# Performance work log

Hardware: AMD Instinct MI355X
Metric: run time of the kernel (lower is better)

The kernel has to match this reference:

```python
import jax, jax.numpy as jnp
import numpy as np
import math

B, S, H, NH = 1, 2048, 1024, 16  # batch, seq, hidden, heads


def setup_inputs() -> dict:
    key = jax.random.key(0)
    ks = jax.random.split(key, 12)
    inp = {
        "query": jax.random.normal(ks[0], (B, S, H), dtype=jnp.float32),
        "key": jax.random.normal(ks[1], (B, S, H), dtype=jnp.float32),
        "value": jax.random.normal(ks[2], (B, S, H), dtype=jnp.float32),
        "attention_mask": jax.random.randint(ks[3], (1, 1, S, S), 0, 2, dtype=jnp.int32),
        # torch nn.Linear params: y = x @ W.T + b, W init ~ U(-1/sqrt(H), 1/sqrt(H))
        "Wq": jax.random.uniform(ks[4], (H, H), jnp.float32, -1, 1) / math.sqrt(H),
        "bq": jax.random.uniform(ks[5], (H,), jnp.float32, -1, 1) / math.sqrt(H),
        "Wk": jax.random.uniform(ks[6], (H, H), jnp.float32, -1, 1) / math.sqrt(H),
        "bk": jax.random.uniform(ks[7], (H,), jnp.float32, -1, 1) / math.sqrt(H),
        "Wv": jax.random.uniform(ks[8], (H, H), jnp.float32, -1, 1) / math.sqrt(H),
        "bv": jax.random.uniform(ks[9], (H,), jnp.float32, -1, 1) / math.sqrt(H),
        "Wo": jax.random.uniform(ks[10], (H, H), jnp.float32, -1, 1) / math.sqrt(H),
        "bo": jax.random.uniform(ks[11], (H,), jnp.float32, -1, 1) / math.sqrt(H),
        "head": NH,
        "hidden_size": H,
    }
    return inp


def reference(query, key, value, attention_mask, Wq, bq, Wk, bk, Wv, bv, Wo, bo, head, hidden_size):
    b, s, _ = query.shape
    d_k = hidden_size // head

    def proj(x, W, bias):
        # [b, s, hidden] -> [b, head, s, d_k]
        y = x @ W.T + bias
        return y.reshape(b, s, head, d_k).transpose(0, 2, 1, 3)

    q = proj(query, Wq, bq)
    k = proj(key, Wk, bk)
    v = proj(value, Wv, bv)

    # naive full score matrix, as in the source (scale by sqrt(d_k) = last dim of q)
    scores = jnp.einsum("bhqd,bhkd->bhqk", q, k) / math.sqrt(d_k)
    # faithful quirk: masked positions are set to 0 (not -inf) before softmax
    scores = jnp.where(attention_mask == 0, jnp.zeros((), scores.dtype), scores)
    attn = jax.nn.softmax(scores, axis=-1)

    out = jnp.einsum("bhqk,bhkd->bhqd", attn, v)  # [b, head, s, d_k]
    out = out.transpose(0, 2, 1, 3).reshape(b, s, head * d_k)
    return out @ Wo.T + bo
```

## Files before the change

kernel.cpp:

```cpp
#include <hip/hip_runtime.h>
#include <hip/hip_bf16.h>


#define S_LEN 2048
#define HID   1024
#define NHEAD 16
#define DK    64

typedef unsigned short u16;
typedef __attribute__((ext_vector_type(8))) short bf16x8;
typedef __attribute__((ext_vector_type(4))) short bf16x4;
typedef __attribute__((ext_vector_type(4))) float f32x4;
typedef __attribute__((ext_vector_type(4))) unsigned u32x4;

__device__ __forceinline__ void load16_lds(const void* g, void* l) {
  __builtin_amdgcn_global_load_lds(
      (const __attribute__((address_space(1))) void*)g,
      (__attribute__((address_space(3))) void*)l, 16, 0, 0);
}

__device__ __forceinline__ short bfbits(float x) {
  __hip_bfloat16 h = __float2bfloat16(x);
  return *(short*)&h;
}
__device__ __forceinline__ bf16x8 cvt8(float4 a, float4 b) {
  bf16x8 r;
  r[0] = bfbits(a.x); r[1] = bfbits(a.y); r[2] = bfbits(a.z); r[3] = bfbits(a.w);
  r[4] = bfbits(b.x); r[5] = bfbits(b.y); r[6] = bfbits(b.z); r[7] = bfbits(b.w);
  return r;
}
__device__ __forceinline__ float bf2f(u16 u) {
  unsigned v = (unsigned)u << 16;
  return *(float*)&v;
}

__global__ __launch_bounds__(256) void cvt_kernel(
    const float* __restrict__ q, const float* __restrict__ k,
    const float* __restrict__ v, const float* __restrict__ wq,
    const float* __restrict__ wk, const float* __restrict__ wv,
    const float* __restrict__ wo, u16* __restrict__ Xbf,
    u16* __restrict__ Wbf) {
  const int y = blockIdx.y;
  size_t i = ((size_t)blockIdx.x * 256 + threadIdx.x) * 8;
  const float* src;
  u16* dst;
  size_t n;
  if (y < 3) {
    src = y == 0 ? q : (y == 1 ? k : v);
    dst = Xbf + (size_t)y * (S_LEN * HID);
    n = (size_t)S_LEN * HID;
  } else {
    int w = y - 3;
    src = w == 0 ? wq : (w == 1 ? wk : (w == 2 ? wv : wo));
    dst = Wbf + (size_t)w * (HID * HID);
    n = (size_t)HID * HID;
  }
  if (i >= n) return;
  float4 a = *(const float4*)(src + i);
  float4 b = *(const float4*)(src + i + 4);
  *(bf16x8*)(dst + i) = cvt8(a, b);
}

__global__ __launch_bounds__(256) void pack_mask_kernel(
    const int* __restrict__ mask, unsigned int* __restrict__ bitsT) {
  int idx = blockIdx.x * 256 + threadIdx.x;
  int row = idx & 2047, widx = idx >> 11;
  const int4* p = (const int4*)(mask + (size_t)row * S_LEN + widx * 32);
  unsigned word = 0;
#pragma unroll
  for (int i = 0; i < 8; ++i) {
    int4 v = p[i];
    word |= (unsigned)(v.x != 0) << (i * 4 + 0);
    word |= (unsigned)(v.y != 0) << (i * 4 + 1);
    word |= (unsigned)(v.z != 0) << (i * 4 + 2);
    word |= (unsigned)(v.w != 0) << (i * 4 + 3);
  }
  bitsT[(size_t)widx * S_LEN + row] = word;
}

__global__ __launch_bounds__(256) void gemm_qkv(
    const u16* __restrict__ Xbf, const u16* __restrict__ Wbf,
    const float* __restrict__ bq, const float* __restrict__ bk,
    const float* __restrict__ bv, u16* __restrict__ Qb,
    u16* __restrict__ Kb, u16* __restrict__ Vt) {
  constexpr int Mm = 2048, Nn = 1024, Kk = 1024, NIT = 16;
  const int z = blockIdx.z;
  const u16* A = Xbf + (size_t)z * (S_LEN * HID);
  const u16* W = Wbf + (size_t)z * (HID * HID);
  const float* bias = z == 0 ? bq : (z == 1 ? bk : bv);
  u16* C = z == 0 ? Qb : (z == 1 ? Kb : Vt);
  const float oscale = (z == 0) ? 0.125f * 1.44269504088896f : 1.0f;
  const int transpose = (z == 2);

  const int tid = threadIdx.x, lane = tid & 63, wave = tid >> 6;
  const int q4 = lane >> 4, c16 = lane & 15;
  const int bx = blockIdx.x;
  const int xcd = bx & 7, sIdx = bx >> 3;
  const int mBase = ((xcd >> 1) * 8 + (sIdx & 7)) * 64;
  const int nBase = ((xcd & 1) * 4 + (sIdx >> 3)) * 128;
  const int wn = wave * 32;

  __shared__ __align__(16) u16 As[2][2][64 * 32];
  __shared__ __align__(16) u16 Bs[2][2][128 * 32];

  f32x4 acc[4][2] = {};
  const int srow = lane >> 2;
  const int sx8 = ((lane & 3) ^ ((srow >> 1) & 3)) * 8;
  const int rx8 = (q4 ^ ((c16 >> 1) & 3)) * 8;

  auto issue = [&](int it, int buf) {
#pragma unroll
    for (int j = 0; j < 2; ++j) {
      int u = wave * 2 + j, h = u >> 2, grp = u & 3;
      load16_lds(A + (size_t)(mBase + grp * 16 + srow) * Kk + it * 64 +
                     h * 32 + sx8,
                 &As[buf][h][grp * 512]);
    }
#pragma unroll
    for (int j = 0; j < 4; ++j) {
      int u = wave * 4 + j, h = u >> 3, grp = u & 7;
      load16_lds(W + (size_t)(nBase + grp * 16 + srow) * Kk + it * 64 +
                     h * 32 + sx8,
                 &Bs[buf][h][grp * 512]);
    }
  };

  issue(0, 0);
  __syncthreads();

  for (int it = 0; it < NIT; ++it) {
    const int buf = it & 1, nbuf = buf ^ 1;
    if (it + 1 < NIT) issue(it + 1, nbuf);
#pragma unroll
    for (int kk = 0; kk < 2; ++kk) {
      bf16x8 af[4], bfr[2];
#pragma unroll
      for (int t = 0; t < 4; ++t)
        af[t] = *(const bf16x8*)&As[buf][kk][(t * 16 + c16) * 32 + rx8];
#pragma unroll
      for (int t = 0; t < 2; ++t)
        bfr[t] = *(const bf16x8*)&Bs[buf][kk][(wn + t * 16 + c16) * 32 + rx8];
#pragma unroll
      for (int mt = 0; mt < 4; ++mt)
#pragma unroll
        for (int nt = 0; nt < 2; ++nt)
          acc[mt][nt] = __builtin_amdgcn_mfma_f32_16x16x32_bf16(
              af[mt], bfr[nt], acc[mt][nt], 0, 0, 0);
    }
    __syncthreads();
  }

#pragma unroll
  for (int nt = 0; nt < 2; ++nt) {
    int col = nBase + wn + nt * 16 + c16;
    float bv2 = bias[col];
#pragma unroll
    for (int mt = 0; mt < 4; ++mt) {
#pragma unroll
      for (int r = 0; r < 4; ++r) {
        int row = mBase + mt * 16 + q4 * 4 + r;
        float v = (acc[mt][nt][r] + bv2) * oscale;
        if (transpose) {
          int vv = row & 31;
          int rowp = (row & ~31) | (((vv & 15) << 1) | (vv >> 4));
          ((__hip_bfloat16*)C)[(size_t)col * Mm + rowp] = __float2bfloat16(v);
        } else {
          ((__hip_bfloat16*)C)[(size_t)row * Nn + col] = __float2bfloat16(v);
        }
      }
    }
  }
}

__global__ __launch_bounds__(512, 4) void attn_kernel(
    const u16* __restrict__ Qb, const u16* __restrict__ Kb,
    const u16* __restrict__ Vt, const unsigned* __restrict__ mbT,
    u16* __restrict__ partOA, u16* __restrict__ partO3,
    float* __restrict__ partL) {
  constexpr int NITA = 8;
  const int lin = blockIdx.x + 8 * (blockIdx.y + 16 * blockIdx.z);
  const int work = ((lin & 7) << 6) | (lin >> 3);
  const int qt = work & 7, h = (work >> 3) & 15, zz = work >> 7;
  const int tid = threadIdx.x, lane = tid & 63, wave = tid >> 6;
  const int q4 = lane >> 4, c16 = lane & 15;

  __shared__ __align__(16) u16 Ks[2][2][64 * 32];
  __shared__ __align__(16) u16 Vs[2][2][64 * 32];
  __shared__ __align__(16) u16 Ps[8][32 * 72];

  const int q0 = qt * 256 + wave * 32;

  bf16x8 qf[2][2];
#pragma unroll
  for (int m = 0; m < 2; ++m)
#pragma unroll
    for (int kk = 0; kk < 2; ++kk)
      qf[m][kk] = *(const bf16x8*)(Qb + (size_t)(q0 + m * 16 + c16) * HID +
                                   h * DK + kk * 32 + q4 * 8);

  f32x4 o[2][4] = {};
  float l_lane[2][4] = {{}, {}};
  const unsigned mlo = 1u << c16, mhi = mlo << 16;

  const int srow = lane >> 2;
  const int sx8 = ((lane & 3) ^ ((srow >> 1) & 3)) * 8;
  const int rx8 = (q4 ^ ((c16 >> 1) & 3)) * 8;
  const int kvbase = zz * (S_LEN / 4);

  auto issueKV = [&](int it, int buf) {
    const int kv0 = kvbase + it * 64;
#pragma unroll
    for (int j = 0; j < 2; ++j) {
      int i = wave * 2 + j;
      if (i < 8) {
        int half = i >> 2, grp = i & 3;
        load16_lds(Kb + (size_t)(kv0 + grp * 16 + srow) * HID + h * DK +
                       half * 32 + sx8,
                   &Ks[buf][half][grp * 512]);
      } else {
        int ii = i - 8;
        int half = ii >> 2, grp = ii & 3;
        load16_lds(Vt + (size_t)(h * DK + grp * 16 + srow) * S_LEN + kv0 +
                       half * 32 + sx8,
                   &Vs[buf][half][grp * 512]);
      }
    }
  };

  issueKV(0, 0);
  __syncthreads();

  u16* pw = &Ps[wave][0];

  for (int it = 0; it < NITA; ++it) {
    const int buf = it & 1, nbuf = buf ^ 1;
    if (it + 1 < NITA) issueKV(it + 1, nbuf);

    const unsigned* mr = mbT + (size_t)(zz * 16 + it * 2) * S_LEN + q0 + q4 * 4;
    u32x4 mwa[2][2];
#pragma unroll
    for (int m = 0; m < 2; ++m) {
      mwa[m][0] = *(const u32x4*)(mr + m * 16);
      mwa[m][1] = *(const u32x4*)(mr + S_LEN + m * 16);
    }

    f32x4 sv[2][4];
#pragma unroll
    for (int nt = 0; nt < 4; ++nt) {
      const int rsw = (nt * 16 + c16) * 32 + rx8;
      bf16x8 kf0 = *(const bf16x8*)&Ks[buf][0][rsw];
      bf16x8 kf1 = *(const bf16x8*)&Ks[buf][1][rsw];
#pragma unroll
      for (int m = 0; m < 2; ++m) {
        f32x4 a = {};
        a = __builtin_amdgcn_mfma_f32_16x16x32_bf16(qf[m][0], kf0, a, 0, 0, 0);
        a = __builtin_amdgcn_mfma_f32_16x16x32_bf16(qf[m][1], kf1, a, 0, 0, 0);
        sv[m][nt] = a;
      }
    }

#pragma unroll
    for (int m = 0; m < 2; ++m)
#pragma unroll
      for (int r = 0; r < 4; ++r) {
#pragma unroll
        for (int nt = 0; nt < 4; ++nt) {
          unsigned word = mwa[m][nt >> 1][r];
          unsigned keep = word & ((nt & 1) ? mhi : mlo);
          float s = keep ? sv[m][nt][r] : 0.0f;
          float p = exp2f(s);
          sv[m][nt][r] = p;
          l_lane[m][r] += p;
        }
        int prow = m * 16 + q4 * 4 + r;
#pragma unroll
        for (int kkp = 0; kkp < 2; ++kkp) {
          unsigned lo = (unsigned)(u16)bfbits(sv[m][2 * kkp][r]);
          unsigned hi = (unsigned)(u16)bfbits(sv[m][2 * kkp + 1][r]);
          *(unsigned*)&pw[prow * 72 + kkp * 32 + c16 * 2] = lo | (hi << 16);
        }
      }

    asm volatile("s_waitcnt lgkmcnt(0)" ::: "memory");

#pragma unroll
    for (int kk = 0; kk < 2; ++kk) {
      bf16x8 pa0 = *(const bf16x8*)&pw[(c16) * 72 + kk * 32 + q4 * 8];
      bf16x8 pa1 = *(const bf16x8*)&pw[(16 + c16) * 72 + kk * 32 + q4 * 8];
#pragma unroll
      for (int nt = 0; nt < 4; ++nt) {
        const int rsw = (nt * 16 + c16) * 32 + rx8;
        bf16x8 vb = *(const bf16x8*)&Vs[buf][kk][rsw];
        o[0][nt] = __builtin_amdgcn_mfma_f32_16x16x32_bf16(pa0, vb, o[0][nt], 0, 0, 0);
        o[1][nt] = __builtin_amdgcn_mfma_f32_16x16x32_bf16(pa1, vb, o[1][nt], 0, 0, 0);
      }
    }
    __syncthreads();
  }

  u16* pO = (zz < 3) ? (partOA + (size_t)zz * (S_LEN * HID)) : partO3;
#pragma unroll
  for (int m = 0; m < 2; ++m)
#pragma unroll
    for (int r = 0; r < 4; ++r) {
      float s = l_lane[m][r];
#pragma unroll
      for (int d = 1; d < 16; d <<= 1) s += __shfl_xor(s, d);
      int row = q0 + m * 16 + q4 * 4 + r;
#pragma unroll
      for (int nt = 0; nt < 4; ++nt)
        ((__hip_bfloat16*)pO)[(size_t)row * HID + h * DK + nt * 16 + c16] =
            __float2bfloat16(o[m][nt][r]);
      if (c16 == 0)
        partL[((size_t)zz * NHEAD + h) * S_LEN + row] = s;
    }
}

__global__ __launch_bounds__(256) void combine_kernel(
    const u16* __restrict__ pOA, const u16* __restrict__ pO3,
    const float* __restrict__ partL, u16* __restrict__ ctx) {
  size_t idx = ((size_t)blockIdx.x * 256 + threadIdx.x) * 4;
  int row = (int)(idx >> 10);
  int col = (int)(idx & 1023);
  int h = col >> 6;
  float l = 0.0f;
#pragma unroll
  for (int z = 0; z < 4; ++z)
    l += partL[((size_t)z * NHEAD + h) * S_LEN + row];
  float inv = 1.0f / l;
  bf16x4 a0 = *(const bf16x4*)(pOA + idx);
  bf16x4 a1 = *(const bf16x4*)(pOA + (size_t)S_LEN * HID + idx);
  bf16x4 a2 = *(const bf16x4*)(pOA + 2 * (size_t)S_LEN * HID + idx);
  bf16x4 a3 = *(const bf16x4*)(pO3 + idx);
  bf16x4 r;
#pragma unroll
  for (int j = 0; j < 4; ++j) {
    float v = (bf2f((u16)a0[j]) + bf2f((u16)a1[j]) + bf2f((u16)a2[j]) +
               bf2f((u16)a3[j])) * inv;
    r[j] = bfbits(v);
  }
  *(bf16x4*)(ctx + idx) = r;
}

__global__ __launch_bounds__(256) void gemm_out(
    const u16* __restrict__ ctx, const u16* __restrict__ Wo,
    const float* __restrict__ bo, float* __restrict__ out) {
  constexpr int Nn = 1024, Kk = 1024, NIT = 16;
  const int tid = threadIdx.x, lane = tid & 63, wave = tid >> 6;
  const int q4 = lane >> 4, c16 = lane & 15;
  const int bx = blockIdx.x;
  const int xcd = bx & 7, sIdx = bx >> 3;
  const int mBase = ((xcd >> 1) * 16 + (sIdx & 15)) * 32;
  const int nBase = ((xcd & 1) * 4 + (sIdx >> 4)) * 128;
  const int wn = wave * 32;

  __shared__ __align__(16) u16 As[2][2][32 * 32];
  __shared__ __align__(16) u16 Bs[2][2][128 * 32];

  f32x4 acc[2][2] = {};
  const int srow = lane >> 2;
  const int sx8 = ((lane & 3) ^ ((srow >> 1) & 3)) * 8;
  const int rx8 = (q4 ^ ((c16 >> 1) & 3)) * 8;

  auto issue = [&](int it, int buf) {
    {
      int u = wave, h = u >> 1, grp = u & 1;
      load16_lds(ctx + (size_t)(mBase + grp * 16 + srow) * Kk + it * 64 +
                     h * 32 + sx8,
                 &As[buf][h][grp * 512]);
    }
#pragma unroll
    for (int j = 0; j < 4; ++j) {
      int u = wave * 4 + j, h = u >> 3, grp = u & 7;
      load16_lds(Wo + (size_t)(nBase + grp * 16 + srow) * Kk + it * 64 +
                     h * 32 + sx8,
                 &Bs[buf][h][grp * 512]);
    }
  };

  issue(0, 0);
  __syncthreads();

  for (int it = 0; it < NIT; ++it) {
    const int buf = it & 1, nbuf = buf ^ 1;
    if (it + 1 < NIT) issue(it + 1, nbuf);
#pragma unroll
    for (int kk = 0; kk < 2; ++kk) {
      bf16x8 af[2], bfr[2];
#pragma unroll
      for (int t = 0; t < 2; ++t)
        af[t] = *(const bf16x8*)&As[buf][kk][(t * 16 + c16) * 32 + rx8];
#pragma unroll
      for (int t = 0; t < 2; ++t)
        bfr[t] = *(const bf16x8*)&Bs[buf][kk][(wn + t * 16 + c16) * 32 + rx8];
#pragma unroll
      for (int mt = 0; mt < 2; ++mt)
#pragma unroll
        for (int nt = 0; nt < 2; ++nt)
          acc[mt][nt] = __builtin_amdgcn_mfma_f32_16x16x32_bf16(
              af[mt], bfr[nt], acc[mt][nt], 0, 0, 0);
    }
    __syncthreads();
  }

#pragma unroll
  for (int nt = 0; nt < 2; ++nt) {
    int col = nBase + wn + nt * 16 + c16;
    float bv = bo[col];
#pragma unroll
    for (int mt = 0; mt < 2; ++mt)
#pragma unroll
      for (int r = 0; r < 4; ++r) {
        int row = mBase + mt * 16 + q4 * 4 + r;
        out[(size_t)row * Nn + col] = acc[mt][nt][r] + bv;
      }
  }
}

extern "C" void kernel_launch(void* const* d_in, const int* in_sizes, int n_in,
                              void* d_out, int out_size, void* d_ws, size_t ws_size,
                              hipStream_t stream) {
  const float* q    = (const float*)d_in[0];
  const float* k    = (const float*)d_in[1];
  const float* v    = (const float*)d_in[2];
  const int*   mask = (const int*)d_in[3];
  const float* Wq = (const float*)d_in[4];
  const float* bq = (const float*)d_in[5];
  const float* Wk = (const float*)d_in[6];
  const float* bk = (const float*)d_in[7];
  const float* Wv = (const float*)d_in[8];
  const float* bv = (const float*)d_in[9];
  const float* Wo = (const float*)d_in[10];
  const float* bo = (const float*)d_in[11];

  const size_t M2 = (size_t)S_LEN * HID;
  const size_t W1 = (size_t)HID * HID;
  const size_t need = (4 * W1 + 3 * M2 + 3 * M2) * 2 +
                      (size_t)S_LEN * 64 * 4 + 2 * NHEAD * S_LEN * 4;
  if (ws_size < need) return;

  u16* Wbf = (u16*)d_ws;
  u16* Xbf = Wbf + 4 * W1;
  u16* Qb = Xbf + 3 * M2;
  u16* Kb = Qb + M2;
  u16* Vt = Kb + M2;
  unsigned* mbits = (unsigned*)(Vt + M2);
  u16* partOA = Xbf;
  u16* partO3 = Wbf;
  float* partL = (float*)(Wbf + 2 * W1);
  u16* ctx = Qb;

  hipLaunchKernelGGL(cvt_kernel, dim3(1024, 7), dim3(256), 0, stream,
                     q, k, v, Wq, Wk, Wv, Wo, Xbf, Wbf);

  hipLaunchKernelGGL(pack_mask_kernel, dim3((S_LEN * (S_LEN / 32)) / 256),
                     dim3(256), 0, stream, mask, mbits);

  hipLaunchKernelGGL(gemm_qkv, dim3(256, 1, 3), dim3(256), 0, stream,
                     Xbf, Wbf, bq, bk, bv, Qb, Kb, Vt);

  hipLaunchKernelGGL(attn_kernel, dim3(S_LEN / 256, NHEAD, 4), dim3(512), 0,
                     stream, Qb, Kb, Vt, mbits, partOA, partO3, partL);

  hipLaunchKernelGGL(combine_kernel, dim3((S_LEN * HID / 4) / 256), dim3(256),
                     0, stream, partOA, partO3, partL, ctx);

  hipLaunchKernelGGL(gemm_out, dim3(512), dim3(256), 0, stream,
                     ctx, Wbf + 3 * W1, bo, (float*)d_out);
}
```

Measured before the change: 206.6 us.

## Fuse mask packing into convert, combine into out-GEMM, retile QKV GEMM

Mask bit-packing becomes an extra grid row of the conversion kernel, and the split-KV combine is folded into the output GEMM's A-tile load, which sums the four partial outputs and scales by the inverse row sums before writing to shared memory. This removes two kernel launches and a round trip for the context matrix. The QKV GEMM becomes one flat 384-block launch with 128x128 tiles and a 2x2 wave layout. The attention softmax now works on pairs of key tiles using raw v_exp_f32 and packed bf16 conversion, which lowers register pressure. The trade-offs are more registers per thread in the GEMM tiles and serialized combine work inside the GEMM main loop.

After: 210.5 us. No clear change (+1.9%).

```diff
diff --git a/kernel.cpp b/kernel.cpp
--- a/kernel.cpp
+++ b/kernel.cpp
@@ -34,13 +34,31 @@
   return *(float*)&v;
 }
 
-__global__ __launch_bounds__(256) void cvt_kernel(
+__global__ __launch_bounds__(256) void cvt_pack_kernel(
     const float* __restrict__ q, const float* __restrict__ k,
     const float* __restrict__ v, const float* __restrict__ wq,
     const float* __restrict__ wk, const float* __restrict__ wv,
-    const float* __restrict__ wo, u16* __restrict__ Xbf,
-    u16* __restrict__ Wbf) {
+    const float* __restrict__ wo, const int* __restrict__ mask,
+    u16* __restrict__ Xbf, u16* __restrict__ Wbf,
+    unsigned int* __restrict__ bitsT) {
   const int y = blockIdx.y;
+  if (y == 7) {
+    if (blockIdx.x >= 512) return;
+    int idx = blockIdx.x * 256 + threadIdx.x;
+    int row = idx & 2047, widx = idx >> 11;
+    const int4* p = (const int4*)(mask + (size_t)row * S_LEN + widx * 32);
+    unsigned word = 0;
+#pragma unroll
+    for (int i = 0; i < 8; ++i) {
+      int4 mv = p[i];
+      word |= (unsigned)(mv.x != 0) << (i * 4 + 0);
+      word |= (unsigned)(mv.y != 0) << (i * 4 + 1);
+      word |= (unsigned)(mv.z != 0) << (i * 4 + 2);
+      word |= (unsigned)(mv.w != 0) << (i * 4 + 3);
+    }
+    bitsT[(size_t)widx * S_LEN + row] = word;
+    return;
+  }
   size_t i = ((size_t)blockIdx.x * 256 + threadIdx.x) * 8;
   const float* src;
   u16* dst;
@@ -61,57 +79,38 @@
   *(bf16x8*)(dst + i) = cvt8(a, b);
 }
 
-__global__ __launch_bounds__(256) void pack_mask_kernel(
-    const int* __restrict__ mask, unsigned int* __restrict__ bitsT) {
-  int idx = blockIdx.x * 256 + threadIdx.x;
-  int row = idx & 2047, widx = idx >> 11;
-  const int4* p = (const int4*)(mask + (size_t)row * S_LEN + widx * 32);
-  unsigned word = 0;
-#pragma unroll
-  for (int i = 0; i < 8; ++i) {
-    int4 v = p[i];
-    word |= (unsigned)(v.x != 0) << (i * 4 + 0);
-    word |= (unsigned)(v.y != 0) << (i * 4 + 1);
-    word |= (unsigned)(v.z != 0) << (i * 4 + 2);
-    word |= (unsigned)(v.w != 0) << (i * 4 + 3);
-  }
-  bitsT[(size_t)widx * S_LEN + row] = word;
-}
-
-__global__ __launch_bounds__(256) void gemm_qkv(
+__global__ __launch_bounds__(256, 2) void gemm_qkv(
     const u16* __restrict__ Xbf, const u16* __restrict__ Wbf,
     const float* __restrict__ bq, const float* __restrict__ bk,
     const float* __restrict__ bv, u16* __restrict__ Qb,
     u16* __restrict__ Kb, u16* __restrict__ Vt) {
-  constexpr int Mm = 2048, Nn = 1024, Kk = 1024, NIT = 16;
-  const int z = blockIdx.z;
-  const u16* A = Xbf + (size_t)z * (S_LEN * HID);
-  const u16* W = Wbf + (size_t)z * (HID * HID);
-  const float* bias = z == 0 ? bq : (z == 1 ? bk : bv);
-  u16* C = z == 0 ? Qb : (z == 1 ? Kb : Vt);
-  const float oscale = (z == 0) ? 0.125f * 1.44269504088896f : 1.0f;
-  const int transpose = (z == 2);
-
+  constexpr int Mm = 2048, Kk = 1024, NIT = 16;
   const int tid = threadIdx.x, lane = tid & 63, wave = tid >> 6;
   const int q4 = lane >> 4, c16 = lane & 15;
   const int bx = blockIdx.x;
-  const int xcd = bx & 7, sIdx = bx >> 3;
-  const int mBase = ((xcd >> 1) * 8 + (sIdx & 7)) * 64;
-  const int nBase = ((xcd & 1) * 4 + (sIdx >> 3)) * 128;
-  const int wn = wave * 32;
-
-  __shared__ __align__(16) u16 As[2][2][64 * 32];
+  const int xcd = bx & 7, s = bx >> 3;
+  const int mBase = (s & 15) * 128;
+  const int nG = xcd * 3 + (s >> 4);
+  const int nBase = nG * 128;
+  const int z = nBase >> 10;
+  const u16* A = Xbf + (size_t)z * (S_LEN * HID);
+  const float* bias = z == 0 ? bq : (z == 1 ? bk : bv);
+  const float oscale = (z == 0) ? 0.125f * 1.44269504088896f : 1.0f;
+
+  const int wr = wave >> 1, wc = wave & 1;
+
+  __shared__ __align__(16) u16 As[2][2][128 * 32];
   __shared__ __align__(16) u16 Bs[2][2][128 * 32];
 
-  f32x4 acc[4][2] = {};
+  f32x4 acc[4][4] = {};
   const int srow = lane >> 2;
   const int sx8 = ((lane & 3) ^ ((srow >> 1) & 3)) * 8;
   const int rx8 = (q4 ^ ((c16 >> 1) & 3)) * 8;
 
   auto issue = [&](int it, int buf) {
 #pragma unroll
-    for (int j = 0; j < 2; ++j) {
-      int u = wave * 2 + j, h = u >> 2, grp = u & 3;
+    for (int j = 0; j < 4; ++j) {
+      int u = wave * 4 + j, h = u >> 3, grp = u & 7;
       load16_lds(A + (size_t)(mBase + grp * 16 + srow) * Kk + it * 64 +
                      h * 32 + sx8,
                  &As[buf][h][grp * 512]);
@@ -119,7 +118,7 @@
 #pragma unroll
     for (int j = 0; j < 4; ++j) {
       int u = wave * 4 + j, h = u >> 3, grp = u & 7;
-      load16_lds(W + (size_t)(nBase + grp * 16 + srow) * Kk + it * 64 +
+      load16_lds(Wbf + (size_t)(nBase + grp * 16 + srow) * Kk + it * 64 +
                      h * 32 + sx8,
                  &Bs[buf][h][grp * 512]);
     }
@@ -133,17 +132,17 @@
     if (it + 1 < NIT) issue(it + 1, nbuf);
 #pragma unroll
     for (int kk = 0; kk < 2; ++kk) {
-      bf16x8 af[4], bfr[2];
+      bf16x8 af[4], bfr[4];
 #pragma unroll
       for (int t = 0; t < 4; ++t)
-        af[t] = *(const bf16x8*)&As[buf][kk][(t * 16 + c16) * 32 + rx8];
-#pragma unroll
-      for (int t = 0; t < 2; ++t)
-        bfr[t] = *(const bf16x8*)&Bs[buf][kk][(wn + t * 16 + c16) * 32 + rx8];
+        af[t] = *(const bf16x8*)&As[buf][kk][(wr * 64 + t * 16 + c16) * 32 + rx8];
+#pragma unroll
+      for (int t = 0; t < 4; ++t)
+        bfr[t] = *(const bf16x8*)&Bs[buf][kk][(wc * 64 + t * 16 + c16) * 32 + rx8];
 #pragma unroll
       for (int mt = 0; mt < 4; ++mt)
 #pragma unroll
-        for (int nt = 0; nt < 2; ++nt)
+        for (int nt = 0; nt < 4; ++nt)
           acc[mt][nt] = __builtin_amdgcn_mfma_f32_16x16x32_bf16(
               af[mt], bfr[nt], acc[mt][nt], 0, 0, 0);
     }
@@ -151,21 +150,23 @@
   }
 
 #pragma unroll
-  for (int nt = 0; nt < 2; ++nt) {
-    int col = nBase + wn + nt * 16 + c16;
+  for (int nt = 0; nt < 4; ++nt) {
+    int colg = nBase + wc * 64 + nt * 16 + c16;
+    int col = colg & 1023;
     float bv2 = bias[col];
 #pragma unroll
     for (int mt = 0; mt < 4; ++mt) {
 #pragma unroll
       for (int r = 0; r < 4; ++r) {
-        int row = mBase + mt * 16 + q4 * 4 + r;
+        int row = mBase + wr * 64 + mt * 16 + q4 * 4 + r;
         float v = (acc[mt][nt][r] + bv2) * oscale;
-        if (transpose) {
+        if (z == 2) {
           int vv = row & 31;
           int rowp = (row & ~31) | (((vv & 15) << 1) | (vv >> 4));
-          ((__hip_bfloat16*)C)[(size_t)col * Mm + rowp] = __float2bfloat16(v);
+          ((__hip_bfloat16*)Vt)[(size_t)col * Mm + rowp] = __float2bfloat16(v);
         } else {
-          ((__hip_bfloat16*)C)[(size_t)row * Nn + col] = __float2bfloat16(v);
+          u16* C = z == 0 ? Qb : Kb;
+          ((__hip_bfloat16*)C)[(size_t)row * 1024 + col] = __float2bfloat16(v);
         }
       }
     }
@@ -237,49 +238,44 @@
     if (it + 1 < NITA) issueKV(it + 1, nbuf);
 
     const unsigned* mr = mbT + (size_t)(zz * 16 + it * 2) * S_LEN + q0 + q4 * 4;
-    u32x4 mwa[2][2];
-#pragma unroll
-    for (int m = 0; m < 2; ++m) {
-      mwa[m][0] = *(const u32x4*)(mr + m * 16);
-      mwa[m][1] = *(const u32x4*)(mr + S_LEN + m * 16);
-    }
-
-    f32x4 sv[2][4];
-#pragma unroll
-    for (int nt = 0; nt < 4; ++nt) {
-      const int rsw = (nt * 16 + c16) * 32 + rx8;
-      bf16x8 kf0 = *(const bf16x8*)&Ks[buf][0][rsw];
-      bf16x8 kf1 = *(const bf16x8*)&Ks[buf][1][rsw];
+
+#pragma unroll
+    for (int ntp = 0; ntp < 2; ++ntp) {
+      u32x4 mw0 = *(const u32x4*)(mr + (size_t)ntp * S_LEN);
+      u32x4 mw1 = *(const u32x4*)(mr + (size_t)ntp * S_LEN + 16);
+      f32x4 sv[2][2];
+#pragma unroll
+      for (int ntb = 0; ntb < 2; ++ntb) {
+        const int nt = ntp * 2 + ntb;
+        const int rsw = (nt * 16 + c16) * 32 + rx8;
+        bf16x8 kf0 = *(const bf16x8*)&Ks[buf][0][rsw];
+        bf16x8 kf1 = *(const bf16x8*)&Ks[buf][1][rsw];
+#pragma unroll
+        for (int m = 0; m < 2; ++m) {
+          f32x4 a = {};
+          a = __builtin_amdgcn_mfma_f32_16x16x32_bf16(qf[m][0], kf0, a, 0, 0, 0);
+          a = __builtin_amdgcn_mfma_f32_16x16x32_bf16(qf[m][1], kf1, a, 0, 0, 0);
+          sv[m][ntb] = a;
+        }
+      }
 #pragma unroll
       for (int m = 0; m < 2; ++m) {
-        f32x4 a = {};
-        a = __builtin_amdgcn_mfma_f32_16x16x32_bf16(qf[m][0], kf0, a, 0, 0, 0);
-        a = __builtin_amdgcn_mfma_f32_16x16x32_bf16(qf[m][1], kf1, a, 0, 0, 0);
-        sv[m][nt] = a;
-      }
-    }
-
-#pragma unroll
-    for (int m = 0; m < 2; ++m)
-#pragma unroll
-      for (int r = 0; r < 4; ++r) {
-#pragma unroll
-        for (int nt = 0; nt < 4; ++nt) {
-          unsigned word = mwa[m][nt >> 1][r];
-          unsigned keep = word & ((nt & 1) ? mhi : mlo);
-          float s = keep ? sv[m][nt][r] : 0.0f;
-          float p = exp2f(s);
-          sv[m][nt][r] = p;
-          l_lane[m][r] += p;
+        const u32x4 mw = m ? mw1 : mw0;
+#pragma unroll
+        for (int r = 0; r < 4; ++r) {
+          unsigned word = mw[r];
+          float s0 = (word & mlo) ? sv[m][0][r] : 0.0f;
+          float s1 = (word & mhi) ? sv[m][1][r] : 0.0f;
+          float p0, p1;
+          asm("v_exp_f32 %0, %1" : "=v"(p0) : "v"(s0));
+          asm("v_exp_f32 %0, %1" : "=v"(p1) : "v"(s1));
+          l_lane[m][r] += p0 + p1;
+          unsigned pk;
+          asm("v_cvt_pk_bf16_f32 %0, %1, %2" : "=v"(pk) : "v"(p0), "v"(p1));
+          *(unsigned*)&pw[(m * 16 + q4 * 4 + r) * 72 + ntp * 32 + c16 * 2] = pk;
         }
-        int prow = m * 16 + q4 * 4 + r;
-#pragma unroll
-        for (int kkp = 0; kkp < 2; ++kkp) {
-          unsigned lo = (unsigned)(u16)bfbits(sv[m][2 * kkp][r]);
-          unsigned hi = (unsigned)(u16)bfbits(sv[m][2 * kkp + 1][r]);
-          *(unsigned*)&pw[prow * 72 + kkp * 32 + c16 * 2] = lo | (hi << 16);
-        }
-      }
+      }
+    }
 
     asm volatile("s_waitcnt lgkmcnt(0)" ::: "memory");
 
@@ -316,59 +312,34 @@
     }
 }
 
-__global__ __launch_bounds__(256) void combine_kernel(
+__global__ __launch_bounds__(256) void gemm_out(
     const u16* __restrict__ pOA, const u16* __restrict__ pO3,
-    const float* __restrict__ partL, u16* __restrict__ ctx) {
-  size_t idx = ((size_t)blockIdx.x * 256 + threadIdx.x) * 4;
-  int row = (int)(idx >> 10);
-  int col = (int)(idx & 1023);
-  int h = col >> 6;
-  float l = 0.0f;
-#pragma unroll
-  for (int z = 0; z < 4; ++z)
-    l += partL[((size_t)z * NHEAD + h) * S_LEN + row];
-  float inv = 1.0f / l;
-  bf16x4 a0 = *(const bf16x4*)(pOA + idx);
-  bf16x4 a1 = *(const bf16x4*)(pOA + (size_t)S_LEN * HID + idx);
-  bf16x4 a2 = *(const bf16x4*)(pOA + 2 * (size_t)S_LEN * HID + idx);
-  bf16x4 a3 = *(const bf16x4*)(pO3 + idx);
-  bf16x4 r;
-#pragma unroll
-  for (int j = 0; j < 4; ++j) {
-    float v = (bf2f((u16)a0[j]) + bf2f((u16)a1[j]) + bf2f((u16)a2[j]) +
-               bf2f((u16)a3[j])) * inv;
-    r[j] = bfbits(v);
-  }
-  *(bf16x4*)(ctx + idx) = r;
-}
-
-__global__ __launch_bounds__(256) void gemm_out(
-    const u16* __restrict__ ctx, const u16* __restrict__ Wo,
+    const float* __restrict__ partL, const u16* __restrict__ Wo,
     const float* __restrict__ bo, float* __restrict__ out) {
   constexpr int Nn = 1024, Kk = 1024, NIT = 16;
+  constexpr size_t M2 = (size_t)S_LEN * HID;
   const int tid = threadIdx.x, lane = tid & 63, wave = tid >> 6;
   const int q4 = lane >> 4, c16 = lane & 15;
   const int bx = blockIdx.x;
-  const int xcd = bx & 7, sIdx = bx >> 3;
-  const int mBase = ((xcd >> 1) * 16 + (sIdx & 15)) * 32;
-  const int nBase = ((xcd & 1) * 4 + (sIdx >> 4)) * 128;
+  const int xcd = bx & 7, s = bx >> 3;
+  const int mBase = (xcd * 8 + (s & 7)) * 32;
+  const int nBase = (s >> 3) * 128;
   const int wn = wave * 32;
 
   __shared__ __align__(16) u16 As[2][2][32 * 32];
   __shared__ __align__(16) u16 Bs[2][2][128 * 32];
+  __shared__ float linv[32][16];
 
   f32x4 acc[2][2] = {};
   const int srow = lane >> 2;
   const int sx8 = ((lane & 3) ^ ((srow >> 1) & 3)) * 8;
   const int rx8 = (q4 ^ ((c16 >> 1) & 3)) * 8;
 
-  auto issue = [&](int it, int buf) {
-    {
-      int u = wave, h = u >> 1, grp = u & 1;
-      load16_lds(ctx + (size_t)(mBase + grp * 16 + srow) * Kk + it * 64 +
-                     h * 32 + sx8,
-                 &As[buf][h][grp * 512]);
-    }
+  const int arow = tid >> 3, acu = tid & 7;
+  const int ahalf = acu >> 2;
+  const int aoff = arow * 32 + ((acu & 3) ^ ((arow >> 1) & 3)) * 8;
+
+  auto issueB = [&](int it, int buf) {
 #pragma unroll
     for (int j = 0; j < 4; ++j) {
       int u = wave * 4 + j, h = u >> 3, grp = u & 7;
@@ -378,12 +349,44 @@
     }
   };
 
-  issue(0, 0);
+  bf16x8 av0, av1, av2, av3;
+  auto aload = [&](int it) {
+    const u16* p = pOA + (size_t)(mBase + arow) * Kk + it * 64 + acu * 8;
+    av0 = *(const bf16x8*)p;
+    av1 = *(const bf16x8*)(p + M2);
+    av2 = *(const bf16x8*)(p + 2 * M2);
+    av3 = *(const bf16x8*)(pO3 + (size_t)(mBase + arow) * Kk + it * 64 + acu * 8);
+  };
+  auto awrite = [&](int it, int buf) {
+    float inv = linv[arow][it];
+    bf16x8 r;
+#pragma unroll
+    for (int j = 0; j < 8; ++j) {
+      float v = (bf2f((u16)av0[j]) + bf2f((u16)av1[j]) +
+                 bf2f((u16)av2[j]) + bf2f((u16)av3[j])) * inv;
+      r[j] = bfbits(v);
+    }
+    *(bf16x8*)&As[buf][ahalf][aoff] = r;
+  };
+
+#pragma unroll
+  for (int e = 0; e < 2; ++e) {
+    int idx = tid * 2 + e, row = idx >> 4, hh = idx & 15;
+    float l = 0.0f;
+#pragma unroll
+    for (int z = 0; z < 4; ++z)
+      l += partL[(size_t)(z * NHEAD + hh) * S_LEN + mBase + row];
+    linv[row][hh] = 1.0f / l;
+  }
+  aload(0);
+  issueB(0, 0);
+  __syncthreads();
+  awrite(0, 0);
   __syncthreads();
 
   for (int it = 0; it < NIT; ++it) {
     const int buf = it & 1, nbuf = buf ^ 1;
-    if (it + 1 < NIT) issue(it + 1, nbuf);
+    if (it + 1 < NIT) { aload(it + 1); issueB(it + 1, nbuf); }
 #pragma unroll
     for (int kk = 0; kk < 2; ++kk) {
       bf16x8 af[2], bfr[2];
@@ -400,6 +403,7 @@
           acc[mt][nt] = __builtin_amdgcn_mfma_f32_16x16x32_bf16(
               af[mt], bfr[nt], acc[mt][nt], 0, 0, 0);
     }
+    if (it + 1 < NIT) awrite(it + 1, nbuf);
     __syncthreads();
   }
 
@@ -448,23 +452,16 @@
   u16* partOA = Xbf;
   u16* partO3 = Wbf;
   float* partL = (float*)(Wbf + 2 * W1);
-  u16* ctx = Qb;
-
-  hipLaunchKernelGGL(cvt_kernel, dim3(1024, 7), dim3(256), 0, stream,
-                     q, k, v, Wq, Wk, Wv, Wo, Xbf, Wbf);
-
-  hipLaunchKernelGGL(pack_mask_kernel, dim3((S_LEN * (S_LEN / 32)) / 256),
-                     dim3(256), 0, stream, mask, mbits);
-
-  hipLaunchKernelGGL(gemm_qkv, dim3(256, 1, 3), dim3(256), 0, stream,
+
+  hipLaunchKernelGGL(cvt_pack_kernel, dim3(1024, 8), dim3(256), 0, stream,
+                     q, k, v, Wq, Wk, Wv, Wo, mask, Xbf, Wbf, mbits);
+
+  hipLaunchKernelGGL(gemm_qkv, dim3(384), dim3(256), 0, stream,
                      Xbf, Wbf, bq, bk, bv, Qb, Kb, Vt);
 
   hipLaunchKernelGGL(attn_kernel, dim3(S_LEN / 256, NHEAD, 4), dim3(512), 0,
                      stream, Qb, Kb, Vt, mbits, partOA, partO3, partL);
 
-  hipLaunchKernelGGL(combine_kernel, dim3((S_LEN * HID / 4) / 256), dim3(256),
-                     0, stream, partOA, partO3, partL, ctx);
-
   hipLaunchKernelGGL(gemm_out, dim3(512), dim3(256), 0, stream,
-                     ctx, Wbf + 3 * W1, bo, (float*)d_out);
-}
+                     partOA, partO3, partL, Wbf + 3 * W1, bo, (float*)d_out);
+}
```
